# Kernel tuning notes

Hardware: AMD Instinct MI355X
Metric: run time of the kernel (lower is better)

## Reference

```python
import jax, jax.numpy as jnp
import numpy as np

B, HH, WW, C = 1, 96, 96, 128
HEADS, K = 4, 7

def setup_inputs() -> dict:
    key = jax.random.key(0)
    ks = jax.random.split(key, 6)
    def lin(k, o, i):
        return jax.random.normal(k, (o, i), jnp.float32) * (1.0 / np.sqrt(i))
    return {
        "x": jax.random.normal(ks[0], (B, HH, WW, C), jnp.float32),
        "qkv_w": lin(ks[1], 3 * C, C),
        "qkv_b": jnp.zeros((3 * C,), jnp.float32),
        "proj_w": lin(ks[2], C, C),
        "proj_b": jnp.zeros((C,), jnp.float32),
        "fc1_w": lin(ks[3], 4 * C, C),
        "fc1_b": jnp.zeros((4 * C,), jnp.float32),
        "fc2_w": lin(ks[4], C, 4 * C),
        "fc2_b": jnp.zeros((C,), jnp.float32),
    }

def _na2d(q, k, v):
    # q,k,v: [B, heads, H, W, hd]; NATTEN 2D neighborhood attention,
    # kernel K, stride 1, dilation 1, non-causal. Windows are clamped at
    # borders so each query attends to exactly K*K in-bounds keys.
    Bq, h, Hs, Ws, hd = q.shape
    start_h = jnp.clip(jnp.arange(Hs) - K // 2, 0, Hs - K)
    idx_h = start_h[:, None] + jnp.arange(K)  # [H, K]
    start_w = jnp.clip(jnp.arange(Ws) - K // 2, 0, Ws - K)
    idx_w = start_w[:, None] + jnp.arange(K)  # [W, K]
    I = idx_h[:, None, :, None]  # -> [H, W, K, K] broadcast
    J = idx_w[None, :, None, :]
    k_nb = k[:, :, I, J, :]  # [B, heads, H, W, K, K, hd]
    v_nb = v[:, :, I, J, :]
    scale = jnp.asarray(hd, q.dtype) ** -0.5
    logits = jnp.einsum('bhijd,bhijkld->bhijkl', q, k_nb) * scale
    attn = jax.nn.softmax(logits.reshape(Bq, h, Hs, Ws, K * K), axis=-1)
    attn = attn.reshape(Bq, h, Hs, Ws, K, K)
    return jnp.einsum('bhijkl,bhijkld->bhijd', attn, v_nb)

def reference(x, qkv_w, qkv_b, proj_w, proj_b, fc1_w, fc1_b, fc2_w, fc2_b):
    Bq, Hs, Ws, Cc = x.shape
    hd = Cc // HEADS
    qkv = x @ qkv_w.T + qkv_b  # [B,H,W,3C]
    q, k, v = jnp.split(qkv, 3, axis=-1)
    def to_heads(t):
        return t.reshape(Bq, Hs, Ws, HEADS, hd).transpose(0, 3, 1, 2, 4)
    o = _na2d(to_heads(q), to_heads(k), to_heads(v))  # [B,heads,H,W,hd]
    o = o.transpose(0, 2, 3, 1, 4).reshape(Bq, Hs, Ws, Cc)
    x0 = o @ proj_w.T + proj_b
    h1 = jax.nn.gelu(x0 @ fc1_w.T + fc1_b, approximate=False)
    return h1 @ fc2_w.T + fc2_b
```

## Files before the change

kernel.cpp:

```cpp
#include <hip/hip_runtime.h>

typedef __bf16 bf16_t;
typedef __bf16 bf16x8 __attribute__((ext_vector_type(8)));
typedef __bf16 bf16x4 __attribute__((ext_vector_type(4)));
typedef float f32x4 __attribute__((ext_vector_type(4)));

#define HH 96
#define WW 96
#define CC 128
#define HD 32
#define KW 7

#define W_PROJ 0
#define W_FC1  16384
#define W_FC2  81920
#define W_TOT  147456

#define PATCH 10
#define PSZ 100
#define NPAD 112
#define STR 136
#define H1S 520

#define R0 0
#define R1 (NPAD * STR)
#define R2 (R1 + 128 * STR)
#define SME (R2 + 16 * STR)

__device__ __forceinline__ bf16x8 cvt8(const float* __restrict__ p) {
    const f32x4 a = *(const f32x4*)p;
    const f32x4 b = *(const f32x4*)(p + 4);
    bf16x8 r;
    r[0] = (bf16_t)a[0]; r[1] = (bf16_t)a[1]; r[2] = (bf16_t)a[2]; r[3] = (bf16_t)a[3];
    r[4] = (bf16_t)b[0]; r[5] = (bf16_t)b[1]; r[6] = (bf16_t)b[2]; r[7] = (bf16_t)b[3];
    return r;
}

template <int NT>
__device__ __forceinline__ void mmaN(const bf16_t* __restrict__ A, int lda,
                                     const bf16_t* __restrict__ W, int ldb,
                                     int K, f32x4* acc) {
    const int lane = threadIdx.x & 63;
    const bf16_t* ap = A + (lane & 15) * lda + ((lane >> 4) * 8);
    const bf16_t* bp = W + (lane & 15) * ldb + ((lane >> 4) * 8);
    for (int k0 = 0; k0 < K; k0 += 32) {
        bf16x8 a = *(const bf16x8*)(ap + k0);
#pragma unroll
        for (int t = 0; t < NT; t++) {
            bf16x8 b = *(const bf16x8*)(bp + t * 16 * ldb + k0);
            acc[t] = __builtin_amdgcn_mfma_f32_16x16x32_bf16(a, b, acc[t], 0, 0, 0);
        }
    }
}

__global__ __launch_bounds__(256) void k_cvt(const float* __restrict__ proj_w,
                                             const float* __restrict__ fc1_w,
                                             const float* __restrict__ fc2_w,
                                             bf16_t* __restrict__ wb) {
    const int idx = blockIdx.x * 256 + threadIdx.x;
    const int base = idx * 4;
    const float* src;
    if (base < W_FC1)      src = proj_w + base;
    else if (base < W_FC2) src = fc1_w + (base - W_FC1);
    else                   src = fc2_w + (base - W_FC2);
    const f32x4 a = *(const f32x4*)src;
    bf16x4 r;
    r[0] = (bf16_t)a[0]; r[1] = (bf16_t)a[1]; r[2] = (bf16_t)a[2]; r[3] = (bf16_t)a[3];
    *(bf16x4*)(wb + base) = r;
}

__global__ __launch_bounds__(256, 2) void k_block(
        const float* __restrict__ x,
        const float* __restrict__ qkv_w, const float* __restrict__ qkv_b,
        const bf16_t* __restrict__ wb,
        const float* __restrict__ proj_b, const float* __restrict__ fc1_b,
        const float* __restrict__ fc2_b,  float* __restrict__ out) {
    __shared__ __align__(16) bf16_t smem[SME];
    bf16_t* ks   = smem + R0;
    bf16_t* vt   = smem + R1;
    bf16_t* qs   = smem + R2;
    bf16_t* Pbuf = smem + R0;
    bf16_t* o_s  = smem + R2;
    bf16_t* x0s  = smem + R0;
    bf16_t* h1s  = smem + R0 + 16 * STR;

    const int tid = threadIdx.x;
    const int w = tid >> 6, lane = tid & 63;
    const int g = lane >> 4, li = lane & 15;
    const int bid = blockIdx.x;
    const int i0 = (bid / 24) * 4, j0 = (bid % 24) * 4;
    const int pr0 = min(max(i0 - 3, 0), HH - PATCH);
    const int pc0 = min(max(j0 - 3, 0), WW - PATCH);
    const int oa = i0 - pr0, ob = j0 - pc0;
    const int head = w;

    {
        const int row = tid >> 1, half = tid & 1;
        *(bf16x8*)(vt + row * STR + NPAD + half * 8) = (bf16x8){0,0,0,0,0,0,0,0};
    }

    float bb6[6];
#pragma unroll
    for (int nt = 0; nt < 6; nt++) bb6[nt] = qkv_b[w * 96 + nt * 16 + li];

    for (int mt = 0; mt < 7; mt++) {
        const int arow = mt * 16 + li;
        const int r99 = min(arow, 99);
        const int pi = r99 / 10, pj = r99 - 10 * pi;
        const float* ax = x + ((pr0 + pi) * WW + (pc0 + pj)) * CC + g * 8;
        bf16x8 a[4];
#pragma unroll
        for (int k0 = 0; k0 < 4; k0++) a[k0] = cvt8(ax + k0 * 32);
#pragma unroll
        for (int nt = 0; nt < 6; nt++) {
            const int n = w * 96 + nt * 16 + li;
            const float* bp = qkv_w + n * CC + g * 8;
            f32x4 acc = {0.f, 0.f, 0.f, 0.f};
#pragma unroll
            for (int k0 = 0; k0 < 4; k0++)
                acc = __builtin_amdgcn_mfma_f32_16x16x32_bf16(a[k0], cvt8(bp + k0 * 32), acc, 0, 0, 0);
            const float bb = bb6[nt];
            const int part = n >> 7, c = n & 127;
            if (part == 0) {
#pragma unroll
                for (int r = 0; r < 4; r++) {
                    const int row = mt * 16 + g * 4 + r;
                    if (row < PSZ) {
                        const int ppi = row / 10, ppj = row - 10 * ppi;
                        const int ta = ppi - oa, tb = ppj - ob;
                        if ((unsigned)ta < 4u && (unsigned)tb < 4u)
                            qs[(ta * 4 + tb) * STR + c] = (bf16_t)(acc[r] + bb);
                    }
                }
            } else if (part == 1) {
#pragma unroll
                for (int r = 0; r < 4; r++)
                    ks[(mt * 16 + g * 4 + r) * STR + c] = (bf16_t)(acc[r] + bb);
            } else {
                bf16x4 pk;
#pragma unroll
                for (int r = 0; r < 4; r++) pk[r] = (bf16_t)(acc[r] + bb);
                *(bf16x4*)(vt + c * STR + mt * 16 + g * 4) = pk;
            }
        }
    }
    __syncthreads();

    f32x4 lg[7];
    {
        const bf16x8 aq = *(const bf16x8*)(qs + li * STR + head * HD + g * 8);
#pragma unroll
        for (int t = 0; t < 7; t++) {
            const bf16x8 bk = *(const bf16x8*)(ks + (t * 16 + li) * STR + head * HD + g * 8);
            lg[t] = __builtin_amdgcn_mfma_f32_16x16x32_bf16(aq, bk, (f32x4){0.f,0.f,0.f,0.f}, 0, 0, 0);
        }
    }
    int lr[4], lc[4];
#pragma unroll
    for (int r = 0; r < 4; r++) {
        const int m = g * 4 + r;
        const int i = i0 + (m >> 2), j = j0 + (m & 3);
        lr[r] = min(max(i - 3, 0), HH - KW) - pr0;
        lc[r] = min(max(j - 3, 0), WW - KW) - pc0;
    }
    const float scale = 0.17677669529663687f;
#pragma unroll
    for (int t = 0; t < 7; t++) {
        const int col = t * 16 + li;
        const int pi = col / 10, pj = col - 10 * pi;
#pragma unroll
        for (int r = 0; r < 4; r++) {
            const bool valid = (col < PSZ) &&
                               ((unsigned)(pi - lr[r]) <= 6u) &&
                               ((unsigned)(pj - lc[r]) <= 6u);
            lg[t][r] = valid ? lg[t][r] * scale : -1e30f;
        }
    }
    f32x4 mx = lg[0], sm;
#pragma unroll
    for (int t = 1; t < 7; t++)
#pragma unroll
        for (int r = 0; r < 4; r++) mx[r] = fmaxf(mx[r], lg[t][r]);
#pragma unroll
    for (int off = 8; off; off >>= 1)
#pragma unroll
        for (int r = 0; r < 4; r++) mx[r] = fmaxf(mx[r], __shfl_xor(mx[r], off));
#pragma unroll
    for (int r = 0; r < 4; r++) sm[r] = 0.f;
#pragma unroll
    for (int t = 0; t < 7; t++)
#pragma unroll
        for (int r = 0; r < 4; r++) {
            lg[t][r] = __expf(lg[t][r] - mx[r]);
            sm[r] += lg[t][r];
        }
#pragma unroll
    for (int off = 8; off; off >>= 1)
#pragma unroll
        for (int r = 0; r < 4; r++) sm[r] += __shfl_xor(sm[r], off);
#pragma unroll
    for (int r = 0; r < 4; r++) sm[r] = 1.f / sm[r];

    __syncthreads();

    bf16_t* Pw = Pbuf + w * 16 * STR;
#pragma unroll
    for (int t = 0; t < 7; t++)
#pragma unroll
        for (int r = 0; r < 4; r++)
            Pw[(g * 4 + r) * STR + t * 16 + li] = (bf16_t)(lg[t][r] * sm[r]);
    *(bf16x4*)(Pw + (lane >> 2) * STR + NPAD + (lane & 3) * 4) = (bf16x4){0,0,0,0};
    __syncthreads();

    f32x4 oA[2] = {};
#pragma unroll
    for (int ks0 = 0; ks0 < 128; ks0 += 32) {
        const bf16x8 a = *(const bf16x8*)(Pw + li * STR + ks0 + g * 8);
#pragma unroll
        for (int t2 = 0; t2 < 2; t2++) {
            const bf16x8 b = *(const bf16x8*)(vt + (head * HD + t2 * 16 + li) * STR + ks0 + g * 8);
            oA[t2] = __builtin_amdgcn_mfma_f32_16x16x32_bf16(a, b, oA[t2], 0, 0, 0);
        }
    }
    __syncthreads();

#pragma unroll
    for (int t2 = 0; t2 < 2; t2++)
#pragma unroll
        for (int r = 0; r < 4; r++)
            o_s[(g * 4 + r) * STR + head * HD + t2 * 16 + li] = (bf16_t)oA[t2][r];
    __syncthreads();

    {
        f32x4 acc[2] = {};
        mmaN<2>(o_s, STR, wb + W_PROJ + (w * 32) * CC, CC, CC, acc);
#pragma unroll
        for (int t = 0; t < 2; t++) {
            const int n = w * 32 + t * 16 + li;
            const float bb = proj_b[n];
#pragma unroll
            for (int r = 0; r < 4; r++)
                x0s[(g * 4 + r) * STR + n] = (bf16_t)(acc[t][r] + bb);
        }
    }
    __syncthreads();

    {
        f32x4 acc[8] = {};
        mmaN<8>(x0s, STR, wb + W_FC1 + (w * 128) * CC, CC, CC, acc);
#pragma unroll
        for (int t = 0; t < 8; t++) {
            const int n = w * 128 + t * 16 + li;
            const float bb = fc1_b[n];
#pragma unroll
            for (int r = 0; r < 4; r++) {
                const int m = g * 4 + r;
                const float xv = acc[t][r] + bb;
                const float u = 0.7978845608028654f * (xv + 0.044715f * xv * xv * xv);
                const float e = __expf(2.f * u);
                const float gg = 0.5f * xv * (2.f - 2.f / (e + 1.f));
                h1s[m * H1S + n] = (bf16_t)gg;
            }
        }
    }
    __syncthreads();

    {
        f32x4 acc[2] = {};
        mmaN<2>(h1s, H1S, wb + W_FC2 + (w * 32) * (4 * CC), 4 * CC, 4 * CC, acc);
#pragma unroll
        for (int t = 0; t < 2; t++) {
            const int n = w * 32 + t * 16 + li;
            const float bb = fc2_b[n];
#pragma unroll
            for (int r = 0; r < 4; r++) {
                const int m = g * 4 + r;
                const int i = i0 + (m >> 2), j = j0 + (m & 3);
                float xv = acc[t][r] + bb;
                xv = fminf(fmaxf(xv, -1e4f), 1e4f);
                out[(i * WW + j) * CC + n] = xv;
            }
        }
    }
}

extern "C" void kernel_launch(void* const* d_in, const int* in_sizes, int n_in,
                              void* d_out, int out_size, void* d_ws, size_t ws_size,
                              hipStream_t stream) {
    const float* x      = (const float*)d_in[0];
    const float* qkv_w  = (const float*)d_in[1];
    const float* qkv_b  = (const float*)d_in[2];
    const float* proj_w = (const float*)d_in[3];
    const float* proj_b = (const float*)d_in[4];
    const float* fc1_w  = (const float*)d_in[5];
    const float* fc1_b  = (const float*)d_in[6];
    const float* fc2_w  = (const float*)d_in[7];
    const float* fc2_b  = (const float*)d_in[8];

    bf16_t* wb = (bf16_t*)d_ws;
    float* out = (float*)d_out;

    k_cvt  <<<144, 256, 0, stream>>>(proj_w, fc1_w, fc2_w, wb);
    k_block<<<576, 256, 0, stream>>>(x, qkv_w, qkv_b, wb,
                                     proj_b, fc1_b, fc2_b, out);
}
```

Measured before the change: 147.3 us.

## Split fused block kernel into separate QKV, attention and MLP kernels

Breaks the single fused kernel, which recomputed QKV for a 10x10 halo patch in every 4x4 tile, into three kernels: a global QKV GEMM writing bf16 q/k/v planes to workspace, an attention+proj kernel that gathers K/V from global memory, and an MLP kernel. This removes the redundant halo QKV recomputation (about 6x overlap) and lowers shared memory use so more blocks fit per CU. In exchange it adds global round trips for q/k/v and x0, two extra launches, and scalar strided gathers for V in the attention kernel.

Result: faster. 123.7 us (-16.0%).

```diff
diff --git a/kernel.cpp b/kernel.cpp
--- a/kernel.cpp
+++ b/kernel.cpp
@@ -9,23 +9,21 @@
 #define WW 96
 #define CC 128
 #define HD 32
+#define TOK (HH * WW)
+#define PLANE (TOK * CC)
 #define KW 7
 
-#define W_PROJ 0
-#define W_FC1  16384
-#define W_FC2  81920
-#define W_TOT  147456
+#define W_QKV  0
+#define W_PROJ 49152
+#define W_FC1  65536
+#define W_FC2  131072
+#define W_TOT  196608
 
 #define PATCH 10
 #define PSZ 100
 #define NPAD 112
 #define STR 136
 #define H1S 520
-
-#define R0 0
-#define R1 (NPAD * STR)
-#define R2 (R1 + 128 * STR)
-#define SME (R2 + 16 * STR)
 
 __device__ __forceinline__ bf16x8 cvt8(const float* __restrict__ p) {
     const f32x4 a = *(const f32x4*)p;
@@ -53,36 +51,63 @@
     }
 }
 
-__global__ __launch_bounds__(256) void k_cvt(const float* __restrict__ proj_w,
+__global__ __launch_bounds__(256) void k_cvt(const float* __restrict__ qkv_w,
+                                             const float* __restrict__ proj_w,
                                              const float* __restrict__ fc1_w,
                                              const float* __restrict__ fc2_w,
                                              bf16_t* __restrict__ wb) {
-    const int idx = blockIdx.x * 256 + threadIdx.x;
-    const int base = idx * 4;
+    const int base = (blockIdx.x * 256 + threadIdx.x) * 4;
     const float* src;
-    if (base < W_FC1)      src = proj_w + base;
-    else if (base < W_FC2) src = fc1_w + (base - W_FC1);
-    else                   src = fc2_w + (base - W_FC2);
+    if (base < W_PROJ)     src = qkv_w  + base;
+    else if (base < W_FC1) src = proj_w + (base - W_PROJ);
+    else if (base < W_FC2) src = fc1_w  + (base - W_FC1);
+    else                   src = fc2_w  + (base - W_FC2);
     const f32x4 a = *(const f32x4*)src;
     bf16x4 r;
     r[0] = (bf16_t)a[0]; r[1] = (bf16_t)a[1]; r[2] = (bf16_t)a[2]; r[3] = (bf16_t)a[3];
     *(bf16x4*)(wb + base) = r;
 }
 
-__global__ __launch_bounds__(256, 2) void k_block(
-        const float* __restrict__ x,
-        const float* __restrict__ qkv_w, const float* __restrict__ qkv_b,
-        const bf16_t* __restrict__ wb,
-        const float* __restrict__ proj_b, const float* __restrict__ fc1_b,
-        const float* __restrict__ fc2_b,  float* __restrict__ out) {
-    __shared__ __align__(16) bf16_t smem[SME];
-    bf16_t* ks   = smem + R0;
-    bf16_t* vt   = smem + R1;
-    bf16_t* qs   = smem + R2;
-    bf16_t* Pbuf = smem + R0;
-    bf16_t* o_s  = smem + R2;
-    bf16_t* x0s  = smem + R0;
-    bf16_t* h1s  = smem + R0 + 16 * STR;
+__global__ __launch_bounds__(256) void k_qkv(const float* __restrict__ x,
+                                             const bf16_t* __restrict__ wb,
+                                             const float* __restrict__ bias,
+                                             bf16_t* __restrict__ qb,
+                                             bf16_t* __restrict__ kb,
+                                             bf16_t* __restrict__ vb) {
+    const int wid = blockIdx.x * 4 + (threadIdx.x >> 6);
+    const int m0 = (wid / 6) * 16;
+    const int n0 = (wid % 6) * 64;
+    const int lane = threadIdx.x & 63;
+    const int g = lane >> 4, li = lane & 15;
+    const float* ap = x + (m0 + li) * CC + g * 8;
+    const bf16_t* bp = wb + W_QKV + (n0 + li) * CC + g * 8;
+    f32x4 acc[4] = {};
+    for (int k0 = 0; k0 < CC; k0 += 32) {
+        bf16x8 a = cvt8(ap + k0);
+#pragma unroll
+        for (int t = 0; t < 4; t++) {
+            bf16x8 b = *(const bf16x8*)(bp + t * 16 * CC + k0);
+            acc[t] = __builtin_amdgcn_mfma_f32_16x16x32_bf16(a, b, acc[t], 0, 0, 0);
+        }
+    }
+#pragma unroll
+    for (int t = 0; t < 4; t++) {
+        const int n = n0 + t * 16 + li;
+        const float bb = bias[n];
+        const int part = n >> 7, c = n & 127;
+        bf16_t* dst = (part == 0) ? qb : (part == 1) ? kb : vb;
+#pragma unroll
+        for (int r = 0; r < 4; r++)
+            dst[(m0 + g * 4 + r) * CC + c] = (bf16_t)(acc[t][r] + bb);
+    }
+}
+
+__global__ __launch_bounds__(256, 4) void k_attn(
+        const bf16_t* __restrict__ qb, const bf16_t* __restrict__ kg,
+        const bf16_t* __restrict__ vg, const bf16_t* __restrict__ wb,
+        const float* __restrict__ proj_b, bf16_t* __restrict__ x0g) {
+    __shared__ __align__(16) bf16_t Pbuf[4 * 16 * STR];
+    __shared__ __align__(16) bf16_t o_s[16 * STR];
 
     const int tid = threadIdx.x;
     const int w = tid >> 6, lane = tid & 63;
@@ -91,67 +116,18 @@
     const int i0 = (bid / 24) * 4, j0 = (bid % 24) * 4;
     const int pr0 = min(max(i0 - 3, 0), HH - PATCH);
     const int pc0 = min(max(j0 - 3, 0), WW - PATCH);
-    const int oa = i0 - pr0, ob = j0 - pc0;
     const int head = w;
-
-    {
-        const int row = tid >> 1, half = tid & 1;
-        *(bf16x8*)(vt + row * STR + NPAD + half * 8) = (bf16x8){0,0,0,0,0,0,0,0};
-    }
-
-    float bb6[6];
-#pragma unroll
-    for (int nt = 0; nt < 6; nt++) bb6[nt] = qkv_b[w * 96 + nt * 16 + li];
-
-    for (int mt = 0; mt < 7; mt++) {
-        const int arow = mt * 16 + li;
-        const int r99 = min(arow, 99);
-        const int pi = r99 / 10, pj = r99 - 10 * pi;
-        const float* ax = x + ((pr0 + pi) * WW + (pc0 + pj)) * CC + g * 8;
-        bf16x8 a[4];
-#pragma unroll
-        for (int k0 = 0; k0 < 4; k0++) a[k0] = cvt8(ax + k0 * 32);
-#pragma unroll
-        for (int nt = 0; nt < 6; nt++) {
-            const int n = w * 96 + nt * 16 + li;
-            const float* bp = qkv_w + n * CC + g * 8;
-            f32x4 acc = {0.f, 0.f, 0.f, 0.f};
-#pragma unroll
-            for (int k0 = 0; k0 < 4; k0++)
-                acc = __builtin_amdgcn_mfma_f32_16x16x32_bf16(a[k0], cvt8(bp + k0 * 32), acc, 0, 0, 0);
-            const float bb = bb6[nt];
-            const int part = n >> 7, c = n & 127;
-            if (part == 0) {
-#pragma unroll
-                for (int r = 0; r < 4; r++) {
-                    const int row = mt * 16 + g * 4 + r;
-                    if (row < PSZ) {
-                        const int ppi = row / 10, ppj = row - 10 * ppi;
-                        const int ta = ppi - oa, tb = ppj - ob;
-                        if ((unsigned)ta < 4u && (unsigned)tb < 4u)
-                            qs[(ta * 4 + tb) * STR + c] = (bf16_t)(acc[r] + bb);
-                    }
-                }
-            } else if (part == 1) {
-#pragma unroll
-                for (int r = 0; r < 4; r++)
-                    ks[(mt * 16 + g * 4 + r) * STR + c] = (bf16_t)(acc[r] + bb);
-            } else {
-                bf16x4 pk;
-#pragma unroll
-                for (int r = 0; r < 4; r++) pk[r] = (bf16_t)(acc[r] + bb);
-                *(bf16x4*)(vt + c * STR + mt * 16 + g * 4) = pk;
-            }
-        }
-    }
-    __syncthreads();
+    const int ch = head * HD;
 
     f32x4 lg[7];
     {
-        const bf16x8 aq = *(const bf16x8*)(qs + li * STR + head * HD + g * 8);
+        const int qi = i0 + (li >> 2), qj = j0 + (li & 3);
+        const bf16x8 aq = *(const bf16x8*)(qb + (qi * WW + qj) * CC + ch + g * 8);
 #pragma unroll
         for (int t = 0; t < 7; t++) {
-            const bf16x8 bk = *(const bf16x8*)(ks + (t * 16 + li) * STR + head * HD + g * 8);
+            const int p = min(t * 16 + li, PSZ - 1);
+            const int pi = p / 10, pj = p - 10 * pi;
+            const bf16x8 bk = *(const bf16x8*)(kg + ((pr0 + pi) * WW + pc0 + pj) * CC + ch + g * 8);
             lg[t] = __builtin_amdgcn_mfma_f32_16x16x32_bf16(aq, bk, (f32x4){0.f,0.f,0.f,0.f}, 0, 0, 0);
         }
     }
@@ -201,8 +177,6 @@
 #pragma unroll
     for (int r = 0; r < 4; r++) sm[r] = 1.f / sm[r];
 
-    __syncthreads();
-
     bf16_t* Pw = Pbuf + w * 16 * STR;
 #pragma unroll
     for (int t = 0; t < 7; t++)
@@ -218,17 +192,21 @@
         const bf16x8 a = *(const bf16x8*)(Pw + li * STR + ks0 + g * 8);
 #pragma unroll
         for (int t2 = 0; t2 < 2; t2++) {
-            const bf16x8 b = *(const bf16x8*)(vt + (head * HD + t2 * 16 + li) * STR + ks0 + g * 8);
+            bf16x8 b;
+#pragma unroll
+            for (int j = 0; j < 8; j++) {
+                const int p = min(ks0 + g * 8 + j, PSZ - 1);
+                const int pi = p / 10, pj = p - 10 * pi;
+                b[j] = vg[((pr0 + pi) * WW + pc0 + pj) * CC + ch + t2 * 16 + li];
+            }
             oA[t2] = __builtin_amdgcn_mfma_f32_16x16x32_bf16(a, b, oA[t2], 0, 0, 0);
         }
     }
-    __syncthreads();
-
 #pragma unroll
     for (int t2 = 0; t2 < 2; t2++)
 #pragma unroll
         for (int r = 0; r < 4; r++)
-            o_s[(g * 4 + r) * STR + head * HD + t2 * 16 + li] = (bf16_t)oA[t2][r];
+            o_s[(g * 4 + r) * STR + ch + t2 * 16 + li] = (bf16_t)oA[t2][r];
     __syncthreads();
 
     {
@@ -239,15 +217,28 @@
             const int n = w * 32 + t * 16 + li;
             const float bb = proj_b[n];
 #pragma unroll
-            for (int r = 0; r < 4; r++)
-                x0s[(g * 4 + r) * STR + n] = (bf16_t)(acc[t][r] + bb);
-        }
-    }
-    __syncthreads();
+            for (int r = 0; r < 4; r++) {
+                const int m = g * 4 + r;
+                const int i = i0 + (m >> 2), j = j0 + (m & 3);
+                x0g[(i * WW + j) * CC + n] = (bf16_t)(acc[t][r] + bb);
+            }
+        }
+    }
+}
+
+__global__ __launch_bounds__(256, 4) void k_mlp(const bf16_t* __restrict__ x0g,
+                                                const bf16_t* __restrict__ wb,
+                                                const float* __restrict__ fc1_b,
+                                                const float* __restrict__ fc2_b,
+                                                float* __restrict__ out) {
+    __shared__ __align__(16) bf16_t h1s[16 * H1S];
+    const int w = threadIdx.x >> 6, lane = threadIdx.x & 63;
+    const int g = lane >> 4, li = lane & 15;
+    const int m0 = blockIdx.x * 16;
 
     {
         f32x4 acc[8] = {};
-        mmaN<8>(x0s, STR, wb + W_FC1 + (w * 128) * CC, CC, CC, acc);
+        mmaN<8>(x0g + m0 * CC, CC, wb + W_FC1 + (w * 128) * CC, CC, CC, acc);
 #pragma unroll
         for (int t = 0; t < 8; t++) {
             const int n = w * 128 + t * 16 + li;
@@ -264,7 +255,6 @@
         }
     }
     __syncthreads();
-
     {
         f32x4 acc[2] = {};
         mmaN<2>(h1s, H1S, wb + W_FC2 + (w * 32) * (4 * CC), 4 * CC, 4 * CC, acc);
@@ -275,10 +265,9 @@
 #pragma unroll
             for (int r = 0; r < 4; r++) {
                 const int m = g * 4 + r;
-                const int i = i0 + (m >> 2), j = j0 + (m & 3);
                 float xv = acc[t][r] + bb;
                 xv = fminf(fmaxf(xv, -1e4f), 1e4f);
-                out[(i * WW + j) * CC + n] = xv;
+                out[(m0 + m) * CC + n] = xv;
             }
         }
     }
@@ -297,10 +286,16 @@
     const float* fc2_w  = (const float*)d_in[7];
     const float* fc2_b  = (const float*)d_in[8];
 
-    bf16_t* wb = (bf16_t*)d_ws;
+    bf16_t* ws = (bf16_t*)d_ws;
+    bf16_t* qb = ws;
+    bf16_t* kb = ws + PLANE;
+    bf16_t* vb = ws + 2 * PLANE;
+    bf16_t* x0 = ws + 3 * PLANE;
+    bf16_t* wb = ws + 4 * PLANE;
     float* out = (float*)d_out;
 
-    k_cvt  <<<144, 256, 0, stream>>>(proj_w, fc1_w, fc2_w, wb);
-    k_block<<<576, 256, 0, stream>>>(x, qkv_w, qkv_b, wb,
-                                     proj_b, fc1_b, fc2_b, out);
-}
+    k_cvt <<<192, 256, 0, stream>>>(qkv_w, proj_w, fc1_w, fc2_w, wb);
+    k_qkv <<<864, 256, 0, stream>>>(x, wb, qkv_b, qb, kb, vb);
+    k_attn<<<576, 256, 0, stream>>>(qb, kb, vb, wb, proj_b, x0);
+    k_mlp <<<576, 256, 0, stream>>>(x0, wb, fc1_b, fc2_b, out);
+}
```
